# Optimization experiments

Measured on AMD Instinct MI355X. Metric: run time of the kernel, lower is better.

## Reference

```python
import jax, jax.numpy as jnp
import numpy as np

N, L, C, H, W, HEAD = 16, 256, 512, 32, 32, 16

def setup_inputs() -> dict:
    key = jax.random.key(0)
    ks = jax.random.split(key, 8)
    s = 0.02  # weight init scale
    return {
        "feature": jax.random.normal(ks[0], (N, C, H, W), jnp.float32),
        "token": jax.random.normal(ks[1], (N, L, C), jnp.float32),
        "wq": jax.random.normal(ks[2], (C, C), jnp.float32) * s,
        "bq": jax.random.normal(ks[3], (C,), jnp.float32) * s,
        "wk": jax.random.normal(ks[4], (C, C), jnp.float32) * s,
        "bk": jax.random.normal(ks[5], (C,), jnp.float32) * s,
        "wv": jax.random.normal(ks[6], (C, C), jnp.float32) * s,
        "bv": jax.random.normal(ks[7], (C,), jnp.float32) * s,
    }

def reference(feature, token, wq, bq, wk, bk, wv, bv):
    n, c, hgt, wid = feature.shape
    h = HEAD
    d = c // h
    l = token.shape[1]
    scale = jnp.asarray(np.sqrt(c / h), feature.dtype)
    tok = token.transpose(0, 2, 1)  # (N, C, L)
    # 1x1 conv projections == per-position GEMMs
    v = (jnp.einsum('ncl,dc->ndl', tok, wv) + bv[None, :, None]).reshape(n, h, d, l)
    k = (jnp.einsum('ncl,dc->ndl', tok, wk) + bk[None, :, None]).reshape(n, h, d, l)
    q = (jnp.einsum('nchw,dc->ndhw', feature, wq) + bq[None, :, None, None])
    q = q.reshape(n, h, d, hgt * wid).transpose(0, 1, 3, 2)  # (N, h, HW, d)
    scores = jnp.einsum('nhqd,nhdl->nhql', q, k) / scale  # (N, h, HW, L)
    coef = jax.nn.softmax(scores, axis=-1)
    proj = jnp.einsum('nhdl,nhql->nhdq', v, coef)  # (N, h, d, HW)
    return feature + proj.reshape(n, c, hgt, wid)
```

## Files before the change

### kernel.cpp

```cpp
#include <hip/hip_runtime.h>
#include <hip/hip_bf16.h>

#define N_ 16
#define L_ 256
#define C_ 512
#define HW_ 1024
#define HEADS_ 16
#define DH_ 32

typedef unsigned short u16;
typedef unsigned int u32;
typedef __attribute__((ext_vector_type(8))) short short8_t;
typedef __attribute__((ext_vector_type(4))) float f32x4;
typedef __attribute__((ext_vector_type(2))) unsigned int u32x2;

__device__ __forceinline__ u16 f2bs(float f) {
    union { float f; u32 i; } x; x.f = f;
    u32 r = x.i + 0x7fffu + ((x.i >> 16) & 1u);
    return (u16)(r >> 16);
}
__device__ __forceinline__ u32 cvt_pk_bf16(float lo, float hi) {
    u32 r;
    asm("v_cvt_pk_bf16_f32 %0, %1, %2" : "=v"(r) : "v"(lo), "v"(hi));
    return r;
}
__device__ __forceinline__ void cvt8(const float* __restrict__ src, void* dst) {
    float4 lo = *(const float4*)src;
    float4 hi = *(const float4*)(src + 4);
    union { u32 w[4]; short8_t v; } pk;
    pk.w[0] = cvt_pk_bf16(lo.x, lo.y);
    pk.w[1] = cvt_pk_bf16(lo.z, lo.w);
    pk.w[2] = cvt_pk_bf16(hi.x, hi.y);
    pk.w[3] = cvt_pk_bf16(hi.z, hi.w);
    *(short8_t*)dst = pk.v;
}
#define AS1(p) (const __attribute__((address_space(1))) void*)(p)
#define AS3(p) (__attribute__((address_space(3))) void*)(p)

__global__ __launch_bounds__(256) void prep_kernel(
    const float* __restrict__ token, const float* __restrict__ wq,
    const float* __restrict__ wk, const float* __restrict__ wv,
    u16* __restrict__ tokb, u16* __restrict__ wqb,
    u16* __restrict__ wkb, u16* __restrict__ wvb)
{
    const int idx = blockIdx.x * 256 + threadIdx.x;
    const float* s; u16* d; int off;
    if (idx < 524288)            { s = token; d = tokb; off = idx; }
    else if (idx < 524288+65536) { s = wq; d = wqb; off = idx - 524288; }
    else if (idx < 524288+131072){ s = wk; d = wkb; off = idx - 524288 - 65536; }
    else                         { s = wv; d = wvb; off = idx - 524288 - 131072; }
    float4 v = ((const float4*)s)[off];
    ushort4 w;
    w.x = f2bs(v.x); w.y = f2bs(v.y); w.z = f2bs(v.z); w.w = f2bs(v.w);
    ((ushort4*)d)[off] = w;
}

__global__ __launch_bounds__(256) void proj_kernel(
    const float* __restrict__ feature,
    const u16* __restrict__ tokb, const u16* __restrict__ wqb,
    const u16* __restrict__ wkb, const u16* __restrict__ wvb,
    const float* __restrict__ bq, const float* __restrict__ bk,
    const float* __restrict__ bv,
    u16* __restrict__ Qout, u16* __restrict__ Kout, u16* __restrict__ Vt)
{
    __shared__ __align__(16) unsigned char smem[36864];

    const int t = threadIdx.x;
    const int lane = t & 63, wid = t >> 6;
    const int i16 = lane & 15, g = lane >> 4;

    if (blockIdx.x < 256) {
        const int xcd = blockIdx.x & 7, j = blockIdx.x >> 3;
        const int m0 = (xcd * 4 + (j & 3)) * 128;
        const int n0 = (j >> 2) * 64;
        u16* Tok = (u16*)smem;
        u16* Bk  = (u16*)(smem + 16384);
        u16* Bv  = (u16*)(smem + 24576);
        u16 (*LTo)[72] = (u16(*)[72])smem;

        const int wm = wid >> 1, wn = wid & 1;
        const int r8 = t >> 3, gr = t & 7;

        f32x4 ak[4][2], av[4][2];
        #pragma unroll
        for (int mt = 0; mt < 4; ++mt)
            #pragma unroll
            for (int nt = 0; nt < 2; ++nt) {
                ak[mt][nt] = (f32x4){0.f, 0.f, 0.f, 0.f};
                av[mt][nt] = (f32x4){0.f, 0.f, 0.f, 0.f};
            }

        for (int c0 = 0; c0 < C_; c0 += 64) {
            __syncthreads();
            #pragma unroll
            for (int p = 0; p < 4; ++p) {
                const int row = p * 32 + r8;
                __builtin_amdgcn_global_load_lds(
                    AS1(tokb + (size_t)(m0 + row) * C_ + c0 + ((gr ^ (row & 7)) << 3)),
                    AS3(smem + (p * 32 + wid * 8) * 128), 16, 0, 0);
            }
            #pragma unroll
            for (int p = 0; p < 2; ++p) {
                const int row = p * 32 + r8;
                const int gs = (gr ^ (row & 7)) << 3;
                __builtin_amdgcn_global_load_lds(
                    AS1(wkb + (size_t)(n0 + row) * C_ + c0 + gs),
                    AS3(smem + 16384 + (p * 32 + wid * 8) * 128), 16, 0, 0);
                __builtin_amdgcn_global_load_lds(
                    AS1(wvb + (size_t)(n0 + row) * C_ + c0 + gs),
                    AS3(smem + 24576 + (p * 32 + wid * 8) * 128), 16, 0, 0);
            }
            __syncthreads();
            #pragma unroll
            for (int ks = 0; ks < 2; ++ks) {
                short8_t a[4], bbk[2], bbv[2];
                #pragma unroll
                for (int mt = 0; mt < 4; ++mt) {
                    const int m = wm * 64 + mt * 16 + i16;
                    a[mt] = *(const short8_t*)&Tok[m * 64 + ((((ks << 2) | g) ^ (m & 7)) << 3)];
                }
                #pragma unroll
                for (int nt = 0; nt < 2; ++nt) {
                    const int d = wn * 32 + nt * 16 + i16;
                    const int sw = d * 64 + ((((ks << 2) | g) ^ (d & 7)) << 3);
                    bbk[nt] = *(const short8_t*)&Bk[sw];
                    bbv[nt] = *(const short8_t*)&Bv[sw];
                }
                #pragma unroll
                for (int mt = 0; mt < 4; ++mt)
                    #pragma unroll
                    for (int nt = 0; nt < 2; ++nt) {
                        ak[mt][nt] = __builtin_amdgcn_mfma_f32_16x16x32_bf16(
                            a[mt], bbk[nt], ak[mt][nt], 0, 0, 0);
                        av[mt][nt] = __builtin_amdgcn_mfma_f32_16x16x32_bf16(
                            a[mt], bbv[nt], av[mt][nt], 0, 0, 0);
                    }
            }
        }
        const int nb = m0 >> 8, l0 = m0 & 255;
        const size_t vtbase = (size_t)nb * C_ * L_;
        #pragma unroll
        for (int nt = 0; nt < 2; ++nt) {
            const int d = n0 + wn * 32 + nt * 16 + i16;
            const float bb = bv[d];
            #pragma unroll
            for (int mt = 0; mt < 4; ++mt) {
                ushort4 w;
                w.x = f2bs(av[mt][nt][0] + bb);
                w.y = f2bs(av[mt][nt][1] + bb);
                w.z = f2bs(av[mt][nt][2] + bb);
                w.w = f2bs(av[mt][nt][3] + bb);
                const int l = l0 + wm * 64 + mt * 16 + g * 4;
                *(ushort4*)&Vt[vtbase + (size_t)d * L_ + l] = w;
            }
        }
        __syncthreads();
        #pragma unroll
        for (int nt = 0; nt < 2; ++nt) {
            const int col = wn * 32 + nt * 16 + i16;
            const float bb = bk[n0 + col];
            #pragma unroll
            for (int mt = 0; mt < 4; ++mt)
                #pragma unroll
                for (int r = 0; r < 4; ++r)
                    LTo[wm * 64 + mt * 16 + g * 4 + r][col] =
                        f2bs(ak[mt][nt][r] + bb);
        }
        __syncthreads();
        #pragma unroll
        for (int rep = 0; rep < 4; ++rep) {
            const int m = (t >> 3) + rep * 32;
            const int cs = (t & 7) * 8;
            *(short8_t*)&Kout[(size_t)(m0 + m) * C_ + n0 + cs] = *(short8_t*)&LTo[m][cs];
        }
    } else {
        const int qid = blockIdx.x - 256;
        const int xcd = qid & 7, j = qid >> 3;
        const int m0 = (xcd * 16 + (j & 15)) * 128;
        const int n0 = (j >> 4) * 128;
        const int n = m0 >> 10, pos0 = m0 & (HW_ - 1);
        u16* Wt = (u16*)smem;
        const int FB = 16384;

        const int wq_pos = wid >> 1, wq_d = wid & 1;
        const int r8 = t >> 3, gr = t & 7;

        f32x4 acc[4][4];
        #pragma unroll
        for (int dm = 0; dm < 4; ++dm)
            #pragma unroll
            for (int pf = 0; pf < 4; ++pf)
                acc[dm][pf] = (f32x4){0.f, 0.f, 0.f, 0.f};

        for (int c0 = 0; c0 < C_; c0 += 64) {
            __syncthreads();
            #pragma unroll
            for (int p = 0; p < 4; ++p) {
                const int row = p * 32 + r8;
                __builtin_amdgcn_global_load_lds(
                    AS1(wqb + (size_t)(n0 + row) * C_ + c0 + ((gr ^ (row & 7)) << 3)),
                    AS3(smem + (p * 32 + wid * 8) * 128), 16, 0, 0);
            }
            #pragma unroll
            for (int p = 0; p < 4; ++p) {
                const int row = p * 16 + (t >> 4);
                const int pos8 = (t & 15) * 8;
                float f8[8];
                *(float4*)&f8[0] = *(const float4*)&feature[
                    ((size_t)n * C_ + c0 + row) * HW_ + pos0 + pos8];
                *(float4*)&f8[4] = *(const float4*)&feature[
                    ((size_t)n * C_ + c0 + row) * HW_ + pos0 + pos8 + 4];
                const int cb = row >> 2, cr = row & 3;
                const int pb = pos8 >> 4, po = (pos8 & 15) * 2;
                cvt8(f8, smem + FB + (cb * 8 + pb) * 160 + cr * 32 + po);
            }
            __syncthreads();
            #pragma unroll
            for (int ks = 0; ks < 2; ++ks) {
                short8_t a[4], b[4];
                #pragma unroll
                for (int dm = 0; dm < 4; ++dm) {
                    const int m = wq_d * 64 + dm * 16 + i16;
                    a[dm] = *(const short8_t*)&Wt[m * 64 + ((((ks << 2) | g) ^ (m & 7)) << 3)];
                }
                #pragma unroll
                for (int pf = 0; pf < 4; ++pf) {
                    const int pb = wq_pos * 4 + pf;
                    const u32 vaddr = FB +
                        (u32)((ks * 8 + g * 2) * 8 + pb) * 160 + (u32)i16 * 2;
                    u32x2 lo, hi;
                    asm volatile("ds_read_b64_tr_b16 %0, %1"
                                 : "=v"(lo) : "v"(vaddr));
                    asm volatile("ds_read_b64_tr_b16 %0, %1 offset:1280"
                                 : "=v"(hi) : "v"(vaddr));
                    union { u32 w[4]; short8_t v; } pk;
                    pk.w[0] = lo[0]; pk.w[1] = lo[1];
                    pk.w[2] = hi[0]; pk.w[3] = hi[1];
                    b[pf] = pk.v;
                }
                asm volatile("s_waitcnt lgkmcnt(0)" ::: "memory");
                __builtin_amdgcn_sched_barrier(0);
                #pragma unroll
                for (int dm = 0; dm < 4; ++dm)
                    #pragma unroll
                    for (int pf = 0; pf < 4; ++pf)
                        acc[dm][pf] = __builtin_amdgcn_mfma_f32_16x16x32_bf16(
                            a[dm], b[pf], acc[dm][pf], 0, 0, 0);
            }
        }
        #pragma unroll
        for (int dm = 0; dm < 4; ++dm) {
            const int dbase = wq_d * 64 + dm * 16 + g * 4;
            float4 b4 = *(const float4*)&bq[n0 + dbase];
            const float bb[4] = {b4.x, b4.y, b4.z, b4.w};
            #pragma unroll
            for (int pf = 0; pf < 4; ++pf) {
                const int pos = wq_pos * 64 + pf * 16 + i16;
                ushort4 w;
                w.x = f2bs(acc[dm][pf][0] + bb[0]);
                w.y = f2bs(acc[dm][pf][1] + bb[1]);
                w.z = f2bs(acc[dm][pf][2] + bb[2]);
                w.w = f2bs(acc[dm][pf][3] + bb[3]);
                *(ushort4*)&Qout[(size_t)(m0 + pos) * C_ + n0 + dbase] = w;
            }
        }
    }
}

__global__ __launch_bounds__(256) void attn_kernel(
    const u16* __restrict__ Qws, const u16* __restrict__ Kws,
    const u16* __restrict__ Vws, const float* __restrict__ feature,
    float* __restrict__ out)
{
    __shared__ __align__(16) unsigned char smem[32768];

    const int t = threadIdx.x;
    const int wid = t >> 6, lane = t & 63;
    const int i16 = lane & 15, g = lane >> 4;
    const int pt = blockIdx.x, h = blockIdx.y, n = blockIdx.z;
    const int pos0 = pt * 64;
    const size_t qbase = ((size_t)n * HW_ + pos0) * C_ + h * DH_;
    const size_t kbase = ((size_t)n * L_) * C_ + h * DH_;
    const size_t vbase = (size_t)n * C_ * L_ + (size_t)h * DH_ * L_;

    const int q = wid * 16 + i16;

    short8_t bq = *(const short8_t*)&Qws[qbase + (size_t)q * C_ + g * 8];

    #pragma unroll
    for (int p = 0; p < 4; ++p) {
        const int kg = (lane & 3) ^ ((lane >> 3) & 3);
        const int kr = wid * 64 + p * 16 + (lane >> 2);
        const u16* ksrc = Kws + kbase + (size_t)kr * C_ + kg * 8;
        __builtin_amdgcn_global_load_lds(AS1(ksrc),
            AS3(smem + wid * 4096 + p * 1024), 16, 0, 0);
        const int vd = wid * 8 + p * 2 + (lane >> 5);
        const u16* vsrc = Vws + vbase + (size_t)vd * L_ + ((lane & 31) ^ (vd & 7)) * 8;
        __builtin_amdgcn_global_load_lds(AS1(vsrc),
            AS3(smem + 16384 + wid * 4096 + p * 1024), 16, 0, 0);
    }
    __syncthreads();

    const int kgr = g ^ ((i16 >> 1) & 3);
    f32x4 s[16];
    #pragma unroll
    for (int nf = 0; nf < 16; ++nf) {
        short8_t a = *(const short8_t*)(smem + (nf * 16 + i16) * 64 + kgr * 16);
        f32x4 z = {0.f, 0.f, 0.f, 0.f};
        s[nf] = __builtin_amdgcn_mfma_f32_16x16x32_bf16(a, bq, z, 0, 0, 0);
    }

    float mm[16], sm[16];
    #pragma unroll
    for (int nf = 0; nf < 16; ++nf)
        mm[nf] = fmaxf(fmaxf(s[nf][0], s[nf][1]), fmaxf(s[nf][2], s[nf][3]));
    #pragma unroll
    for (int st = 8; st >= 1; st >>= 1)
        #pragma unroll
        for (int i = 0; i < 8; ++i)
            if (i < st) mm[i] = fmaxf(mm[i], mm[i + st]);
    float m = mm[0];
    m = fmaxf(m, __shfl_xor(m, 16));
    m = fmaxf(m, __shfl_xor(m, 32));

    const float K2 = 0.25506288f;
    #pragma unroll
    for (int nf = 0; nf < 16; ++nf) {
        #pragma unroll
        for (int r = 0; r < 4; ++r) s[nf][r] = exp2f((s[nf][r] - m) * K2);
        sm[nf] = (s[nf][0] + s[nf][1]) + (s[nf][2] + s[nf][3]);
    }
    #pragma unroll
    for (int st = 8; st >= 1; st >>= 1)
        #pragma unroll
        for (int i = 0; i < 8; ++i)
            if (i < st) sm[i] += sm[i + st];
    float ssum = sm[0];
    ssum += __shfl_xor(ssum, 16);
    ssum += __shfl_xor(ssum, 32);
    const float pinv = 1.0f / ssum;

    __syncthreads();

    f32x4 o0 = {0.f, 0.f, 0.f, 0.f}, o1 = {0.f, 0.f, 0.f, 0.f};
    const int e7 = i16 & 7;

    #pragma unroll
    for (int hb = 0; hb < 2; ++hb) {
        #pragma unroll
        for (int nfp = 0; nfp < 8; ++nfp) {
            const int nf = hb * 8 + nfp;
            #pragma unroll
            for (int w = 0; w < 2; ++w) {
                u32 pw = cvt_pk_bf16(s[nf][2 * w] * pinv, s[nf][2 * w + 1] * pinv);
                const int gran = (nfp * 2 + (g >> 1)) ^ e7;
                *(u32*)(smem + q * 256 + gran * 16 + ((g & 1) * 2 + w) * 4) = pw;
            }
        }
        __syncthreads();
        #pragma unroll
        for (int ks = 0; ks < 4; ++ks) {
            short8_t pb = *(const short8_t*)(smem + q * 256 + (((ks * 4 + g) ^ e7) * 16));
            const int vg = (((hb * 4 + ks) * 4 + g) ^ e7) * 16;
            short8_t va0 = *(const short8_t*)(smem + 16384 + i16 * 512 + vg);
            short8_t va1 = *(const short8_t*)(smem + 16384 + (16 + i16) * 512 + vg);
            o0 = __builtin_amdgcn_mfma_f32_16x16x32_bf16(va0, pb, o0, 0, 0, 0);
            o1 = __builtin_amdgcn_mfma_f32_16x16x32_bf16(va1, pb, o1, 0, 0, 0);
        }
        if (hb == 0) __syncthreads();
    }

    const size_t obase = ((size_t)n * C_ + h * DH_) * HW_ + pos0 + q;
    #pragma unroll
    for (int r = 0; r < 4; ++r) {
        const size_t oa = obase + (size_t)(g * 4 + r) * HW_;
        out[oa] = feature[oa] + o0[r];
        const size_t ob = obase + (size_t)(16 + g * 4 + r) * HW_;
        out[ob] = feature[ob] + o1[r];
    }
}

extern "C" void kernel_launch(void* const* d_in, const int* in_sizes, int n_in,
                              void* d_out, int out_size, void* d_ws, size_t ws_size,
                              hipStream_t stream)
{
    const float* feature = (const float*)d_in[0];
    const float* token   = (const float*)d_in[1];
    const float* wq      = (const float*)d_in[2];
    const float* bq      = (const float*)d_in[3];
    const float* wk      = (const float*)d_in[4];
    const float* bk      = (const float*)d_in[5];
    const float* wv      = (const float*)d_in[6];
    const float* bv      = (const float*)d_in[7];
    float* out = (float*)d_out;

    u16* Qws = (u16*)d_ws;
    u16* Kws = Qws + (size_t)N_ * HW_ * C_;
    u16* Vws = Kws + (size_t)N_ * L_ * C_;

    char* ob = (char*)d_out;
    u16* tokb = (u16*)(ob + (16u << 20));
    u16* wqb  = (u16*)(ob + (20u << 20));
    u16* wkb  = (u16*)(ob + (20u << 20) + 524288);
    u16* wvb  = (u16*)(ob + (20u << 20) + 1048576);

    prep_kernel<<<dim3(2816), 256, 0, stream>>>(token, wq, wk, wv,
                                                tokb, wqb, wkb, wvb);
    proj_kernel<<<dim3(768), 256, 0, stream>>>(feature, tokb, wqb, wkb, wvb,
                                               bq, bk, bv, Qws, Kws, Vws);
    attn_kernel<<<dim3(16, 16, 16), 256, 0, stream>>>(Qws, Kws, Vws, feature, out);
}
```

Baseline: 76.32 us.

## Pre-transpose feature to bf16 position-major and unify Q GEMM with K/V tiling

The prep kernel now also converts feature to bf16 and transposes it into a position-major layout in scratch space inside the output buffer, using an LDS transpose tile. The Q projection then loads it with async global-to-LDS copies like the K/V path, uses 128x64 tiles (more blocks), and stages output through LDS for coalesced stores. This removes the in-loop fp32 loads, conversion and transposed LDS reads from the GEMM. In exchange it adds an extra write and read of the bf16 feature through global memory.

```diff
diff --git a/kernel.cpp b/kernel.cpp
--- a/kernel.cpp
+++ b/kernel.cpp
@@ -12,7 +12,6 @@
 typedef unsigned int u32;
 typedef __attribute__((ext_vector_type(8))) short short8_t;
 typedef __attribute__((ext_vector_type(4))) float f32x4;
-typedef __attribute__((ext_vector_type(2))) unsigned int u32x2;
 
 __device__ __forceinline__ u16 f2bs(float f) {
     union { float f; u32 i; } x; x.f = f;
@@ -24,50 +23,73 @@
     asm("v_cvt_pk_bf16_f32 %0, %1, %2" : "=v"(r) : "v"(lo), "v"(hi));
     return r;
 }
-__device__ __forceinline__ void cvt8(const float* __restrict__ src, void* dst) {
-    float4 lo = *(const float4*)src;
-    float4 hi = *(const float4*)(src + 4);
-    union { u32 w[4]; short8_t v; } pk;
-    pk.w[0] = cvt_pk_bf16(lo.x, lo.y);
-    pk.w[1] = cvt_pk_bf16(lo.z, lo.w);
-    pk.w[2] = cvt_pk_bf16(hi.x, hi.y);
-    pk.w[3] = cvt_pk_bf16(hi.z, hi.w);
-    *(short8_t*)dst = pk.v;
-}
 #define AS1(p) (const __attribute__((address_space(1))) void*)(p)
 #define AS3(p) (__attribute__((address_space(3))) void*)(p)
 
 __global__ __launch_bounds__(256) void prep_kernel(
     const float* __restrict__ token, const float* __restrict__ wq,
     const float* __restrict__ wk, const float* __restrict__ wv,
+    const float* __restrict__ feature,
     u16* __restrict__ tokb, u16* __restrict__ wqb,
-    u16* __restrict__ wkb, u16* __restrict__ wvb)
+    u16* __restrict__ wkb, u16* __restrict__ wvb,
+    u16* __restrict__ Ftb)
 {
-    const int idx = blockIdx.x * 256 + threadIdx.x;
-    const float* s; u16* d; int off;
-    if (idx < 524288)            { s = token; d = tokb; off = idx; }
-    else if (idx < 524288+65536) { s = wq; d = wqb; off = idx - 524288; }
-    else if (idx < 524288+131072){ s = wk; d = wkb; off = idx - 524288 - 65536; }
-    else                         { s = wv; d = wvb; off = idx - 524288 - 131072; }
-    float4 v = ((const float4*)s)[off];
-    ushort4 w;
-    w.x = f2bs(v.x); w.y = f2bs(v.y); w.z = f2bs(v.z); w.w = f2bs(v.w);
-    ((ushort4*)d)[off] = w;
-}
-
-__global__ __launch_bounds__(256) void proj_kernel(
-    const float* __restrict__ feature,
-    const u16* __restrict__ tokb, const u16* __restrict__ wqb,
-    const u16* __restrict__ wkb, const u16* __restrict__ wvb,
+    __shared__ float LT[64][67];
+    const int t = threadIdx.x;
+
+    if (blockIdx.x < 2816) {
+        const int idx = blockIdx.x * 256 + t;
+        const float* s; u16* d; int off;
+        if (idx < 524288)            { s = token; d = tokb; off = idx; }
+        else if (idx < 524288+65536) { s = wq; d = wqb; off = idx - 524288; }
+        else if (idx < 524288+131072){ s = wk; d = wkb; off = idx - 524288 - 65536; }
+        else                         { s = wv; d = wvb; off = idx - 524288 - 131072; }
+        float4 v = ((const float4*)s)[off];
+        ushort4 w;
+        w.x = f2bs(v.x); w.y = f2bs(v.y); w.z = f2bs(v.z); w.w = f2bs(v.w);
+        ((ushort4*)d)[off] = w;
+    } else {
+        const int tidx = blockIdx.x - 2816;
+        const int pb = tidx & 15, cb = (tidx >> 4) & 7, n = tidx >> 7;
+        const int c0 = cb * 64, pos0 = pb * 64;
+
+        #pragma unroll
+        for (int r = 0; r < 4; ++r) {
+            const int c = r * 16 + (t >> 4);
+            const int p = (t & 15) * 4;
+            float4 v = *(const float4*)&feature[
+                ((size_t)n * C_ + c0 + c) * HW_ + pos0 + p];
+            LT[c][p] = v.x; LT[c][p+1] = v.y; LT[c][p+2] = v.z; LT[c][p+3] = v.w;
+        }
+        __syncthreads();
+        #pragma unroll
+        for (int rep = 0; rep < 2; ++rep) {
+            const int pos = (t >> 3) + rep * 32;
+            const int c = (t & 7) * 8;
+            u16 tmp[8];
+            #pragma unroll
+            for (int j = 0; j < 8; ++j) tmp[j] = f2bs(LT[c + j][pos]);
+            *(short8_t*)&Ftb[(size_t)(n * HW_ + pos0 + pos) * C_ + c0 + c] =
+                *(short8_t*)tmp;
+        }
+    }
+}
+
+__global__ __launch_bounds__(256) void gemm_kernel(
+    const u16* __restrict__ Ftb, const u16* __restrict__ tokb,
+    const u16* __restrict__ wqb, const u16* __restrict__ wkb,
+    const u16* __restrict__ wvb,
     const float* __restrict__ bq, const float* __restrict__ bk,
     const float* __restrict__ bv,
     u16* __restrict__ Qout, u16* __restrict__ Kout, u16* __restrict__ Vt)
 {
-    __shared__ __align__(16) unsigned char smem[36864];
+    __shared__ __align__(16) unsigned char smem[32768];
 
     const int t = threadIdx.x;
     const int lane = t & 63, wid = t >> 6;
     const int i16 = lane & 15, g = lane >> 4;
+    const int wm = wid >> 1, wn = wid & 1;
+    const int r8 = t >> 3, gr = t & 7;
 
     if (blockIdx.x < 256) {
         const int xcd = blockIdx.x & 7, j = blockIdx.x >> 3;
@@ -77,9 +99,6 @@
         u16* Bk  = (u16*)(smem + 16384);
         u16* Bv  = (u16*)(smem + 24576);
         u16 (*LTo)[72] = (u16(*)[72])smem;
-
-        const int wm = wid >> 1, wn = wid & 1;
-        const int r8 = t >> 3, gr = t & 7;
 
         f32x4 ak[4][2], av[4][2];
         #pragma unroll
@@ -163,8 +182,7 @@
             for (int mt = 0; mt < 4; ++mt)
                 #pragma unroll
                 for (int r = 0; r < 4; ++r)
-                    LTo[wm * 64 + mt * 16 + g * 4 + r][col] =
-                        f2bs(ak[mt][nt][r] + bb);
+                    LTo[wm * 64 + mt * 16 + g * 4 + r][col] = f2bs(ak[mt][nt][r] + bb);
         }
         __syncthreads();
         #pragma unroll
@@ -177,20 +195,17 @@
         const int qid = blockIdx.x - 256;
         const int xcd = qid & 7, j = qid >> 3;
         const int m0 = (xcd * 16 + (j & 15)) * 128;
-        const int n0 = (j >> 4) * 128;
-        const int n = m0 >> 10, pos0 = m0 & (HW_ - 1);
-        u16* Wt = (u16*)smem;
-        const int FB = 16384;
-
-        const int wq_pos = wid >> 1, wq_d = wid & 1;
-        const int r8 = t >> 3, gr = t & 7;
-
-        f32x4 acc[4][4];
-        #pragma unroll
-        for (int dm = 0; dm < 4; ++dm)
-            #pragma unroll
-            for (int pf = 0; pf < 4; ++pf)
-                acc[dm][pf] = (f32x4){0.f, 0.f, 0.f, 0.f};
+        const int n0 = (j >> 4) * 64;
+        u16* Ft = (u16*)smem;
+        u16* Bq = (u16*)(smem + 16384);
+        u16 (*LTo)[72] = (u16(*)[72])smem;
+
+        f32x4 aq[4][2];
+        #pragma unroll
+        for (int mt = 0; mt < 4; ++mt)
+            #pragma unroll
+            for (int nt = 0; nt < 2; ++nt)
+                aq[mt][nt] = (f32x4){0.f, 0.f, 0.f, 0.f};
 
         for (int c0 = 0; c0 < C_; c0 += 64) {
             __syncthreads();
@@ -198,71 +213,55 @@
             for (int p = 0; p < 4; ++p) {
                 const int row = p * 32 + r8;
                 __builtin_amdgcn_global_load_lds(
+                    AS1(Ftb + (size_t)(m0 + row) * C_ + c0 + ((gr ^ (row & 7)) << 3)),
+                    AS3(smem + (p * 32 + wid * 8) * 128), 16, 0, 0);
+            }
+            #pragma unroll
+            for (int p = 0; p < 2; ++p) {
+                const int row = p * 32 + r8;
+                __builtin_amdgcn_global_load_lds(
                     AS1(wqb + (size_t)(n0 + row) * C_ + c0 + ((gr ^ (row & 7)) << 3)),
-                    AS3(smem + (p * 32 + wid * 8) * 128), 16, 0, 0);
-            }
-            #pragma unroll
-            for (int p = 0; p < 4; ++p) {
-                const int row = p * 16 + (t >> 4);
-                const int pos8 = (t & 15) * 8;
-                float f8[8];
-                *(float4*)&f8[0] = *(const float4*)&feature[
-                    ((size_t)n * C_ + c0 + row) * HW_ + pos0 + pos8];
-                *(float4*)&f8[4] = *(const float4*)&feature[
-                    ((size_t)n * C_ + c0 + row) * HW_ + pos0 + pos8 + 4];
-                const int cb = row >> 2, cr = row & 3;
-                const int pb = pos8 >> 4, po = (pos8 & 15) * 2;
-                cvt8(f8, smem + FB + (cb * 8 + pb) * 160 + cr * 32 + po);
+                    AS3(smem + 16384 + (p * 32 + wid * 8) * 128), 16, 0, 0);
             }
             __syncthreads();
             #pragma unroll
             for (int ks = 0; ks < 2; ++ks) {
-                short8_t a[4], b[4];
-                #pragma unroll
-                for (int dm = 0; dm < 4; ++dm) {
-                    const int m = wq_d * 64 + dm * 16 + i16;
-                    a[dm] = *(const short8_t*)&Wt[m * 64 + ((((ks << 2) | g) ^ (m & 7)) << 3)];
+                short8_t a[4], b[2];
+                #pragma unroll
+                for (int mt = 0; mt < 4; ++mt) {
+                    const int m = wm * 64 + mt * 16 + i16;
+                    a[mt] = *(const short8_t*)&Ft[m * 64 + ((((ks << 2) | g) ^ (m & 7)) << 3)];
                 }
                 #pragma unroll
-                for (int pf = 0; pf < 4; ++pf) {
-                    const int pb = wq_pos * 4 + pf;
-                    const u32 vaddr = FB +
-                        (u32)((ks * 8 + g * 2) * 8 + pb) * 160 + (u32)i16 * 2;
-                    u32x2 lo, hi;
-                    asm volatile("ds_read_b64_tr_b16 %0, %1"
-                                 : "=v"(lo) : "v"(vaddr));
-                    asm volatile("ds_read_b64_tr_b16 %0, %1 offset:1280"
-                                 : "=v"(hi) : "v"(vaddr));
-                    union { u32 w[4]; short8_t v; } pk;
-                    pk.w[0] = lo[0]; pk.w[1] = lo[1];
-                    pk.w[2] = hi[0]; pk.w[3] = hi[1];
-                    b[pf] = pk.v;
+                for (int nt = 0; nt < 2; ++nt) {
+                    const int d = wn * 32 + nt * 16 + i16;
+                    b[nt] = *(const short8_t*)&Bq[d * 64 + ((((ks << 2) | g) ^ (d & 7)) << 3)];
                 }
-                asm volatile("s_waitcnt lgkmcnt(0)" ::: "memory");
-                __builtin_amdgcn_sched_barrier(0);
-                #pragma unroll
-                for (int dm = 0; dm < 4; ++dm)
+                #pragma unroll
+                for (int mt = 0; mt < 4; ++mt)
                     #pragma unroll
-                    for (int pf = 0; pf < 4; ++pf)
-                        acc[dm][pf] = __builtin_amdgcn_mfma_f32_16x16x32_bf16(
-                            a[dm], b[pf], acc[dm][pf], 0, 0, 0);
-            }
-        }
-        #pragma unroll
-        for (int dm = 0; dm < 4; ++dm) {
-            const int dbase = wq_d * 64 + dm * 16 + g * 4;
-            float4 b4 = *(const float4*)&bq[n0 + dbase];
-            const float bb[4] = {b4.x, b4.y, b4.z, b4.w};
-            #pragma unroll
-            for (int pf = 0; pf < 4; ++pf) {
-                const int pos = wq_pos * 64 + pf * 16 + i16;
-                ushort4 w;
-                w.x = f2bs(acc[dm][pf][0] + bb[0]);
-                w.y = f2bs(acc[dm][pf][1] + bb[1]);
-                w.z = f2bs(acc[dm][pf][2] + bb[2]);
-                w.w = f2bs(acc[dm][pf][3] + bb[3]);
-                *(ushort4*)&Qout[(size_t)(m0 + pos) * C_ + n0 + dbase] = w;
-            }
+                    for (int nt = 0; nt < 2; ++nt)
+                        aq[mt][nt] = __builtin_amdgcn_mfma_f32_16x16x32_bf16(
+                            a[mt], b[nt], aq[mt][nt], 0, 0, 0);
+            }
+        }
+        __syncthreads();
+        #pragma unroll
+        for (int nt = 0; nt < 2; ++nt) {
+            const int col = wn * 32 + nt * 16 + i16;
+            const float bb = bq[n0 + col];
+            #pragma unroll
+            for (int mt = 0; mt < 4; ++mt)
+                #pragma unroll
+                for (int r = 0; r < 4; ++r)
+                    LTo[wm * 64 + mt * 16 + g * 4 + r][col] = f2bs(aq[mt][nt][r] + bb);
+        }
+        __syncthreads();
+        #pragma unroll
+        for (int rep = 0; rep < 4; ++rep) {
+            const int m = (t >> 3) + rep * 32;
+            const int cs = (t & 7) * 8;
+            *(short8_t*)&Qout[(size_t)(m0 + m) * C_ + n0 + cs] = *(short8_t*)&LTo[m][cs];
         }
     }
 }
@@ -399,14 +398,15 @@
     u16* Vws = Kws + (size_t)N_ * L_ * C_;
 
     char* ob = (char*)d_out;
+    u16* Ftb  = (u16*)ob;
     u16* tokb = (u16*)(ob + (16u << 20));
-    u16* wqb  = (u16*)(ob + (20u << 20));
-    u16* wkb  = (u16*)(ob + (20u << 20) + 524288);
-    u16* wvb  = (u16*)(ob + (20u << 20) + 1048576);
-
-    prep_kernel<<<dim3(2816), 256, 0, stream>>>(token, wq, wk, wv,
-                                                tokb, wqb, wkb, wvb);
-    proj_kernel<<<dim3(768), 256, 0, stream>>>(feature, tokb, wqb, wkb, wvb,
-                                               bq, bk, bv, Qws, Kws, Vws);
+    u16* wkb  = (u16*)(ob + (20u << 20));
+    u16* wvb  = (u16*)(ob + (20u << 20) + 524288);
+    u16* wqb  = (u16*)(ob + (21u << 20));
+
+    prep_kernel<<<dim3(4864), 256, 0, stream>>>(token, wq, wk, wv, feature,
+                                                tokb, wqb, wkb, wvb, Ftb);
+    gemm_kernel<<<dim3(1280), 256, 0, stream>>>(Ftb, tokb, wqb, wkb, wvb,
+                                                bq, bk, bv, Qws, Kws, Vws);
     attn_kernel<<<dim3(16, 16, 16), 256, 0, stream>>>(Qws, Kws, Vws, feature, out);
 }
```

After: 71.04 us, median of 2. -6.9%, faster.
